# Performance work log

Measured on AMD Instinct MI355X. Metric: run time of the kernel, lower is better.

Reference implementation:

```python
import jax, jax.numpy as jnp
import numpy as np

EMB = 768
HEADS = 12
HEAD_DIM = EMB // HEADS

def setup_inputs() -> dict:
    key = jax.random.key(0)
    ks = jax.random.split(key, 5)
    B, T = 8, 1024
    x = jax.random.normal(ks[0], (B, T, EMB), dtype=jnp.float32)
    s = 1.0 / np.sqrt(EMB)
    W_attn = jax.random.normal(ks[1], (EMB, 3 * EMB), dtype=jnp.float32) * s
    b_attn = jax.random.normal(ks[2], (3 * EMB,), dtype=jnp.float32) * 0.02
    W_proj = jax.random.normal(ks[3], (EMB, EMB), dtype=jnp.float32) * s
    b_proj = jax.random.normal(ks[4], (EMB,), dtype=jnp.float32) * 0.02
    return {"x": x, "W_attn": W_attn, "b_attn": b_attn, "W_proj": W_proj, "b_proj": b_proj}

def reference(x, W_attn, b_attn, W_proj, b_proj):
    B, T, C = x.shape
    qkv = x @ W_attn + b_attn  # [B,T,3C]
    q, k, v = jnp.split(qkv, 3, axis=-1)
    # [B,H,T,d]
    q = q.reshape(B, T, HEADS, HEAD_DIM).transpose(0, 2, 1, 3)
    k = k.reshape(B, T, HEADS, HEAD_DIM).transpose(0, 2, 1, 3)
    v = v.reshape(B, T, HEADS, HEAD_DIM).transpose(0, 2, 1, 3)
    scores = jnp.einsum('bhqd,bhkd->bhqk', q, k) * (HEAD_DIM ** -0.5)
    causal = jnp.tril(jnp.ones((T, T), dtype=bool))
    scores = jnp.where(causal[None, None], scores, -jnp.inf)
    attn = jax.nn.softmax(scores, axis=-1)
    out = jnp.einsum('bhqk,bhkd->bhqd', attn, v)
    out = out.transpose(0, 2, 1, 3).reshape(B, T, C)
    return out @ W_proj + b_proj
```

## Files before the change

### kernel.cpp

```cpp
#include <hip/hip_runtime.h>
#include <hip/hip_bf16.h>

typedef __bf16 bf16;
typedef __attribute__((ext_vector_type(8))) __bf16 bf16x8;
typedef __attribute__((ext_vector_type(4))) short s16x4;
typedef __attribute__((ext_vector_type(4))) float f32x4;

#define EMB 768
#define T_SEQ 1024
#define HEADS 12
#define HDIM 64

__global__ void prep_k(const float* __restrict__ x, bf16* __restrict__ xb,
                       const float* __restrict__ Wa, bf16* __restrict__ Wta,
                       const float* __restrict__ Wp, bf16* __restrict__ Wtp) {
  __shared__ float tile[32][33];
  const int blk = blockIdx.x, tid = threadIdx.x;
  if (blk < 3072) {
    const size_t i = (size_t)blk * 256 + tid;
    const float4* p = (const float4*)(x + i * 8);
    const float4 a = p[0], b = p[1];
    bf16x8 v;
    v[0] = (bf16)a.x; v[1] = (bf16)a.y; v[2] = (bf16)a.z; v[3] = (bf16)a.w;
    v[4] = (bf16)b.x; v[5] = (bf16)b.y; v[6] = (bf16)b.z; v[7] = (bf16)b.w;
    *(bf16x8*)(xb + i * 8) = v;
    return;
  }
  const float* in;
  bf16* out;
  int C, t;
  if (blk < 3072 + 1728) { in = Wa; out = Wta; C = 3 * EMB; t = blk - 3072; }
  else                   { in = Wp; out = Wtp; C = EMB;     t = blk - 4800; }
  const int R = EMB;
  const int c0 = (t % (C / 32)) * 32, r0 = (t / (C / 32)) * 32;
  const int tx = tid & 31, ty = tid >> 5;
  for (int i = ty; i < 32; i += 8)
    tile[i][tx] = in[(size_t)(r0 + i) * C + c0 + tx];
  __syncthreads();
  for (int i = ty; i < 32; i += 8)
    out[(size_t)(c0 + i) * R + r0 + tx] = (bf16)tile[tx][i];
}

template <int MODE>
__global__ __launch_bounds__(256) void gemm_bt(
    const bf16* __restrict__ A, const bf16* __restrict__ Bt, const float* __restrict__ bias,
    bf16* __restrict__ Cb, float* __restrict__ Cf, int M, int N, int K) {
  __shared__ __align__(16) bf16 As0[128 * 32];
  __shared__ __align__(16) bf16 As1[128 * 32];
  __shared__ __align__(16) bf16 Bs0[128 * 32];
  __shared__ __align__(16) bf16 Bs1[128 * 32];
  const int lane = threadIdx.x & 63;
  const int wave = threadIdx.x >> 6;
  const int quad = lane >> 4, lc = lane & 15;
  const int m0 = blockIdx.y * 128, n0 = blockIdx.x * 128;
  const int wm = (wave >> 1) * 64, wn = (wave & 1) * 64;
  const int srow = lane >> 2;
  const int skk = (lane & 3) * 8;

  f32x4 zero = {0.f, 0.f, 0.f, 0.f};
  f32x4 acc[4][4];
#pragma unroll
  for (int i = 0; i < 4; ++i)
#pragma unroll
    for (int j = 0; j < 4; ++j) acc[i][j] = zero;

  for (int k0 = 0; k0 < K; k0 += 64) {
    __syncthreads();
#pragma unroll
    for (int c = wave; c < 8; c += 4) {
      const bf16* gA = A + (size_t)(m0 + c * 16 + srow) * K + k0 + skk;
      const bf16* gB = Bt + (size_t)(n0 + c * 16 + srow) * K + k0 + skk;
      __builtin_amdgcn_global_load_lds((const __attribute__((address_space(1))) void*)gA,
                                       (__attribute__((address_space(3))) void*)(As0 + c * 512), 16, 0, 0);
      __builtin_amdgcn_global_load_lds((const __attribute__((address_space(1))) void*)(gA + 32),
                                       (__attribute__((address_space(3))) void*)(As1 + c * 512), 16, 0, 0);
      __builtin_amdgcn_global_load_lds((const __attribute__((address_space(1))) void*)gB,
                                       (__attribute__((address_space(3))) void*)(Bs0 + c * 512), 16, 0, 0);
      __builtin_amdgcn_global_load_lds((const __attribute__((address_space(1))) void*)(gB + 32),
                                       (__attribute__((address_space(3))) void*)(Bs1 + c * 512), 16, 0, 0);
    }
    __syncthreads();
    {
      bf16x8 af[4], bfr[4];
#pragma unroll
      for (int t = 0; t < 4; ++t) af[t] = *(const bf16x8*)&As0[(wm + t * 16 + lc) * 32 + quad * 8];
#pragma unroll
      for (int t = 0; t < 4; ++t) bfr[t] = *(const bf16x8*)&Bs0[(wn + t * 16 + lc) * 32 + quad * 8];
#pragma unroll
      for (int tm = 0; tm < 4; ++tm)
#pragma unroll
        for (int tn = 0; tn < 4; ++tn)
          acc[tm][tn] = __builtin_amdgcn_mfma_f32_16x16x32_bf16(af[tm], bfr[tn], acc[tm][tn], 0, 0, 0);
    }
    {
      bf16x8 af[4], bfr[4];
#pragma unroll
      for (int t = 0; t < 4; ++t) af[t] = *(const bf16x8*)&As1[(wm + t * 16 + lc) * 32 + quad * 8];
#pragma unroll
      for (int t = 0; t < 4; ++t) bfr[t] = *(const bf16x8*)&Bs1[(wn + t * 16 + lc) * 32 + quad * 8];
#pragma unroll
      for (int tm = 0; tm < 4; ++tm)
#pragma unroll
        for (int tn = 0; tn < 4; ++tn)
          acc[tm][tn] = __builtin_amdgcn_mfma_f32_16x16x32_bf16(af[tm], bfr[tn], acc[tm][tn], 0, 0, 0);
    }
  }

#pragma unroll
  for (int tm = 0; tm < 4; ++tm) {
#pragma unroll
    for (int tn = 0; tn < 4; ++tn) {
      const int col = n0 + wn + tn * 16 + lc;
      const float bv = bias[col];
#pragma unroll
      for (int r = 0; r < 4; ++r) {
        const int row = m0 + wm + tm * 16 + quad * 4 + r;
        const float v = acc[tm][tn][r] + bv;
        if (MODE == 0) Cb[(size_t)row * N + col] = (bf16)v;
        else           Cf[(size_t)row * N + col] = v;
      }
    }
  }
}

__global__ __launch_bounds__(512, 4) void attn_k(const bf16* __restrict__ qkv,
                                                 bf16* __restrict__ outb) {
  __shared__ __align__(16) bf16 Qs[128][72];
  __shared__ __align__(16) bf16 Ks[128][72];
  __shared__ __align__(16) bf16 Vt[64][132];

  const int lane = threadIdx.x & 63;
  const int wave = threadIdx.x >> 6;
  const int quad = lane >> 4, lc = lane & 15;
  const int flat = blockIdx.x;
  const int bh = flat % (HEADS * 8);
  const int qt = 7 - flat / (HEADS * 8);
  const int h = bh % HEADS;
  const int b = bh / HEADS;
  const int q0 = qt * 128;
  const size_t rowB = (size_t)b * T_SEQ;
  const int hoff = h * HDIM;
  const int tid = threadIdx.x;

  for (int c = tid; c < 128 * 8; c += 512) {
    const int r = c >> 3, d8 = (c & 7) * 8;
    *(bf16x8*)&Qs[r][d8] = *(const bf16x8*)(qkv + (rowB + q0 + r) * (3 * EMB) + hoff + d8);
  }

  f32x4 zero = {0.f, 0.f, 0.f, 0.f};
  float m_run = -1e30f, l_run = 0.f;
  f32x4 o[4];
#pragma unroll
  for (int dt = 0; dt < 4; ++dt) o[dt] = zero;
  const int myq = q0 + wave * 16 + lc;

  for (int kt = 0; kt <= qt; ++kt) {
    const int kb = kt * 128;
    __syncthreads();
    for (int c = tid; c < 128 * 8; c += 512) {
      const int key = c >> 3, d8 = (c & 7) * 8;
      *(bf16x8*)&Ks[key][d8] =
          *(const bf16x8*)(qkv + (rowB + kb + key) * (3 * EMB) + EMB + hoff + d8);
    }
    for (int c = tid; c < 128 * 8; c += 512) {
      const int key = c >> 3, d8 = (c & 7) * 8;
      bf16x8 v = *(const bf16x8*)(qkv + (rowB + kb + key) * (3 * EMB) + 2 * EMB + hoff + d8);
#pragma unroll
      for (int i = 0; i < 8; ++i) Vt[d8 + i][key] = v[i];
    }
    __syncthreads();

    f32x4 s[8];
#pragma unroll
    for (int j = 0; j < 8; ++j) s[j] = zero;
#pragma unroll
    for (int ks = 0; ks < 2; ++ks) {
      bf16x8 bq = *(const bf16x8*)&Qs[wave * 16 + lc][ks * 32 + quad * 8];
#pragma unroll
      for (int j = 0; j < 8; ++j) {
        bf16x8 ak = *(const bf16x8*)&Ks[j * 16 + lc][ks * 32 + quad * 8];
        s[j] = __builtin_amdgcn_mfma_f32_16x16x32_bf16(ak, bq, s[j], 0, 0, 0);
      }
    }

    const bool diag = (kt == qt);
    float mloc = -1e30f;
#pragma unroll
    for (int j = 0; j < 8; ++j) {
#pragma unroll
      for (int r = 0; r < 4; ++r) {
        float v = s[j][r] * 0.125f;
        if (diag && (kb + j * 16 + quad * 4 + r > myq)) v = -1e30f;
        s[j][r] = v;
        mloc = fmaxf(mloc, v);
      }
    }
    mloc = fmaxf(mloc, __shfl_xor(mloc, 16));
    mloc = fmaxf(mloc, __shfl_xor(mloc, 32));

    const float mnew = fmaxf(m_run, mloc);
    const float alpha = __expf(m_run - mnew);
    m_run = mnew;

    s16x4 pf[8];
    float rsum = 0.f;
#pragma unroll
    for (int j = 0; j < 8; ++j) {
#pragma unroll
      for (int r = 0; r < 4; ++r) {
        const float p = __expf(s[j][r] - mnew);
        rsum += p;
        pf[j][r] = __builtin_bit_cast(short, (bf16)p);
      }
    }
    rsum += __shfl_xor(rsum, 16);
    rsum += __shfl_xor(rsum, 32);
    l_run = l_run * alpha + rsum;
#pragma unroll
    for (int dt = 0; dt < 4; ++dt)
#pragma unroll
      for (int r = 0; r < 4; ++r) o[dt][r] *= alpha;

#pragma unroll
    for (int j = 0; j < 8; ++j) {
#pragma unroll
      for (int dt = 0; dt < 4; ++dt) {
        s16x4 av = *(const s16x4*)&Vt[dt * 16 + lc][j * 16 + quad * 4];
        o[dt] = __builtin_amdgcn_mfma_f32_16x16x16bf16_1k(av, pf[j], o[dt], 0, 0, 0);
      }
    }
  }

  const float inv = 1.0f / l_run;
  __syncthreads();
#pragma unroll
  for (int dt = 0; dt < 4; ++dt)
#pragma unroll
    for (int r = 0; r < 4; ++r)
      Qs[wave * 16 + lc][dt * 16 + quad * 4 + r] = (bf16)(o[dt][r] * inv);
  __syncthreads();
  for (int c = tid; c < 128 * 8; c += 512) {
    const int r = c >> 3, d8 = (c & 7) * 8;
    *(bf16x8*)(outb + (rowB + q0 + r) * EMB + hoff + d8) = *(const bf16x8*)&Qs[r][d8];
  }
}

extern "C" void kernel_launch(void* const* d_in, const int* in_sizes, int n_in,
                              void* d_out, int out_size, void* d_ws, size_t ws_size,
                              hipStream_t stream) {
  const float* x = (const float*)d_in[0];
  const float* Wattn = (const float*)d_in[1];
  const float* battn = (const float*)d_in[2];
  const float* Wproj = (const float*)d_in[3];
  const float* bproj = (const float*)d_in[4];
  float* out = (float*)d_out;

  const int M = in_sizes[0] / EMB;
  const int Bn = M / T_SEQ;

  bf16* ws = (bf16*)d_ws;
  bf16* xb = ws;
  bf16* Wt_attn = xb + (size_t)M * EMB;
  bf16* Wt_proj = Wt_attn + (size_t)3 * EMB * EMB;
  bf16* qkv = Wt_proj + (size_t)EMB * EMB;
  bf16* attnb = qkv + (size_t)M * 3 * EMB;

  const int cvt_blocks = M * EMB / 8 / 256;
  prep_k<<<cvt_blocks + 1728 + 576, 256, 0, stream>>>(x, xb, Wattn, Wt_attn, Wproj, Wt_proj);

  gemm_bt<0><<<dim3(3 * EMB / 128, M / 128), 256, 0, stream>>>(
      xb, Wt_attn, battn, qkv, nullptr, M, 3 * EMB, EMB);

  attn_k<<<dim3((T_SEQ / 128) * Bn * HEADS), 512, 0, stream>>>(qkv, attnb);

  gemm_bt<1><<<dim3(EMB / 128, M / 128), 256, 0, stream>>>(
      attnb, Wt_proj, bproj, nullptr, out, M, EMB, EMB);
}
```

Before: 181.2 us.

## Pre-transpose V in a separate kernel and use exp2 softmax

Adds a kernel that transposes V per head into a [bh][d][T] global buffer, so the attention kernel loads V^T tiles with vector loads instead of scattering scalar bf16 writes into shared memory on every key tile. The Vt row pitch grows from 132 to 136 so 16-byte stores stay aligned. Softmax now folds log2(e) into the score scale and uses exp2f, which saves a multiply per exponent. The cost is an extra kernel launch plus a full write and re-read of V through global memory.

Measured after the change: 195.8 us. 8.1% more time.

```diff
diff --git a/kernel.cpp b/kernel.cpp
--- a/kernel.cpp
+++ b/kernel.cpp
@@ -1,5 +1,6 @@
 #include <hip/hip_runtime.h>
 #include <hip/hip_bf16.h>
+#include <math.h>
 
 typedef __bf16 bf16;
 typedef __attribute__((ext_vector_type(8))) __bf16 bf16x8;
@@ -39,6 +40,27 @@
   __syncthreads();
   for (int i = ty; i < 32; i += 8)
     out[(size_t)(c0 + i) * R + r0 + tx] = (bf16)tile[tx][i];
+}
+
+__global__ __launch_bounds__(256) void vtr_k(const bf16* __restrict__ qkv, bf16* __restrict__ vtg) {
+  __shared__ bf16 tile[64][68];
+  const int tb = blockIdx.x * 64;
+  const int bh = blockIdx.y;
+  const int b = bh / HEADS, h = bh % HEADS;
+  const size_t base = (size_t)b * T_SEQ * (3 * EMB) + 2 * EMB + h * HDIM;
+  const int tid = threadIdx.x;
+  for (int c = tid; c < 64 * 8; c += 256) {
+    const int r = c >> 3, d8 = (c & 7) * 8;
+    *(bf16x8*)&tile[r][d8] = *(const bf16x8*)(qkv + base + (size_t)(tb + r) * (3 * EMB) + d8);
+  }
+  __syncthreads();
+  for (int c = tid; c < 64 * 8; c += 256) {
+    const int d = c >> 3, t8 = (c & 7) * 8;
+    bf16x8 v;
+#pragma unroll
+    for (int i = 0; i < 8; ++i) v[i] = tile[t8 + i][d];
+    *(bf16x8*)(vtg + (((size_t)bh * HDIM + d) << 10) + tb + t8) = v;
+  }
 }
 
 template <int MODE>
@@ -124,10 +146,11 @@
 }
 
 __global__ __launch_bounds__(512, 4) void attn_k(const bf16* __restrict__ qkv,
+                                                 const bf16* __restrict__ vtg,
                                                  bf16* __restrict__ outb) {
   __shared__ __align__(16) bf16 Qs[128][72];
   __shared__ __align__(16) bf16 Ks[128][72];
-  __shared__ __align__(16) bf16 Vt[64][132];
+  __shared__ __align__(16) bf16 Vt[64][136];
 
   const int lane = threadIdx.x & 63;
   const int wave = threadIdx.x >> 6;
@@ -141,6 +164,7 @@
   const size_t rowB = (size_t)b * T_SEQ;
   const int hoff = h * HDIM;
   const int tid = threadIdx.x;
+  const float C1 = 0.125f * 1.44269504f;
 
   for (int c = tid; c < 128 * 8; c += 512) {
     const int r = c >> 3, d8 = (c & 7) * 8;
@@ -162,11 +186,10 @@
       *(bf16x8*)&Ks[key][d8] =
           *(const bf16x8*)(qkv + (rowB + kb + key) * (3 * EMB) + EMB + hoff + d8);
     }
-    for (int c = tid; c < 128 * 8; c += 512) {
-      const int key = c >> 3, d8 = (c & 7) * 8;
-      bf16x8 v = *(const bf16x8*)(qkv + (rowB + kb + key) * (3 * EMB) + 2 * EMB + hoff + d8);
-#pragma unroll
-      for (int i = 0; i < 8; ++i) Vt[d8 + i][key] = v[i];
+    for (int c = tid; c < 64 * 16; c += 512) {
+      const int dd = c >> 4, kc = (c & 15) * 8;
+      *(bf16x8*)&Vt[dd][kc] =
+          *(const bf16x8*)(vtg + (((size_t)bh * HDIM + dd) << 10) + kb + kc);
     }
     __syncthreads();
 
@@ -189,7 +212,7 @@
     for (int j = 0; j < 8; ++j) {
 #pragma unroll
       for (int r = 0; r < 4; ++r) {
-        float v = s[j][r] * 0.125f;
+        float v = s[j][r] * C1;
         if (diag && (kb + j * 16 + quad * 4 + r > myq)) v = -1e30f;
         s[j][r] = v;
         mloc = fmaxf(mloc, v);
@@ -199,7 +222,7 @@
     mloc = fmaxf(mloc, __shfl_xor(mloc, 32));
 
     const float mnew = fmaxf(m_run, mloc);
-    const float alpha = __expf(m_run - mnew);
+    const float alpha = exp2f(m_run - mnew);
     m_run = mnew;
 
     s16x4 pf[8];
@@ -208,7 +231,7 @@
     for (int j = 0; j < 8; ++j) {
 #pragma unroll
       for (int r = 0; r < 4; ++r) {
-        const float p = __expf(s[j][r] - mnew);
+        const float p = exp2f(s[j][r] - mnew);
         rsum += p;
         pf[j][r] = __builtin_bit_cast(short, (bf16)p);
       }
@@ -263,7 +286,8 @@
   bf16* Wt_attn = xb + (size_t)M * EMB;
   bf16* Wt_proj = Wt_attn + (size_t)3 * EMB * EMB;
   bf16* qkv = Wt_proj + (size_t)EMB * EMB;
-  bf16* attnb = qkv + (size_t)M * 3 * EMB;
+  bf16* vtg = qkv + (size_t)M * 3 * EMB;
+  bf16* attnb = vtg + (size_t)M * EMB;
 
   const int cvt_blocks = M * EMB / 8 / 256;
   prep_k<<<cvt_blocks + 1728 + 576, 256, 0, stream>>>(x, xb, Wattn, Wt_attn, Wproj, Wt_proj);
@@ -271,7 +295,9 @@
   gemm_bt<0><<<dim3(3 * EMB / 128, M / 128), 256, 0, stream>>>(
       xb, Wt_attn, battn, qkv, nullptr, M, 3 * EMB, EMB);
 
-  attn_k<<<dim3((T_SEQ / 128) * Bn * HEADS), 512, 0, stream>>>(qkv, attnb);
+  vtr_k<<<dim3(T_SEQ / 64, Bn * HEADS), 256, 0, stream>>>(qkv, vtg);
+
+  attn_k<<<dim3((T_SEQ / 128) * Bn * HEADS), 512, 0, stream>>>(qkv, vtg, attnb);
 
   gemm_bt<1><<<dim3(EMB / 128, M / 128), 256, 0, stream>>>(
       attnb, Wt_proj, bproj, nullptr, out, M, EMB, EMB);
```
